# Kernel optimization log

Hardware: AMD Instinct MI355X
Metric: run time of the kernel (lower is better)

## Reference

```python
import jax, jax.numpy as jnp
import numpy as np

B, F, H, E, V, T = 128, 2048, 1024, 512, 16384, 20
TEMP = 1.0


def setup_inputs() -> dict:
    key = jax.random.key(0)
    ks = jax.random.split(key, 12)
    sc = lambda i, shape, s=0.02: jax.random.normal(ks[i], shape, jnp.float32) * s
    # Gumbel(0,1) noise for RelaxedOneHotCategorical.rsample
    u = jax.random.uniform(ks[11], (T, B, V), jnp.float32, 1e-6, 1.0 - 1e-6)
    gumbel = -jnp.log(-jnp.log(u))
    return dict(
        image_features=jax.random.normal(ks[0], (B, F), jnp.float32),
        agent_w=sc(1, (H, F)),
        agent_b=jnp.zeros((H,), jnp.float32),
        w_ih=sc(2, (3 * H, E)),
        w_hh=sc(3, (3 * H, H)),
        b_ih=jnp.zeros((3 * H,), jnp.float32),
        b_hh=jnp.zeros((3 * H,), jnp.float32),
        w_out=sc(4, (V, H)),
        b_out=jnp.zeros((V,), jnp.float32),
        emb_w=sc(5, (E, V)),
        sos=sc(6, (E,), 0.01),
        gumbel=gumbel,
    )


def _gru_cell(x, h, w_ih, w_hh, b_ih, b_hh):
    # torch.nn.GRUCell math
    gi = x @ w_ih.T + b_ih          # [B, 3H]
    gh = h @ w_hh.T + b_hh          # [B, 3H]
    i_r, i_z, i_n = jnp.split(gi, 3, axis=-1)
    h_r, h_z, h_n = jnp.split(gh, 3, axis=-1)
    r = jax.nn.sigmoid(i_r + h_r)
    z = jax.nn.sigmoid(i_z + h_z)
    n = jnp.tanh(i_n + r * h_n)
    return (1.0 - z) * n + z * h


def reference(image_features, agent_w, agent_b, w_ih, w_hh, b_ih, b_hh,
              w_out, b_out, emb_w, sos, gumbel):
    h0 = image_features @ agent_w.T + agent_b                 # agent: [B, H]
    e0 = jnp.broadcast_to(sos, (image_features.shape[0], sos.shape[0]))  # SOS embed

    def step(carry, g_t):
        h, e = carry
        h = _gru_cell(e, h, w_ih, w_hh, b_ih, b_hh)            # [B, H]
        logits = h @ w_out.T + b_out                           # [B, V]
        # Gumbel-softmax sample (training mode, not straight-through)
        x = jax.nn.softmax((logits + g_t) / TEMP, axis=-1)     # [B, V]
        e = x @ emb_w.T                                        # soft-one-hot embedding, [B, E]
        return (h, e), x

    _, seq = jax.lax.scan(step, (h0, e0), gumbel)              # [T, B, V]
    return jnp.transpose(seq, (1, 0, 2))                       # [B, T, V]
```

## Files before the change

### kernel.cpp

```cpp
#include <hip/hip_runtime.h>
#include <hip/hip_bf16.h>
#include <math.h>

namespace {

constexpr int kB = 128, kF = 2048, kH = 1024, kE = 512, kV = 16384, kT = 20;

typedef __attribute__((ext_vector_type(4))) float f32x4;
typedef __attribute__((ext_vector_type(8))) short bf16x8;

#define MFMA(a, b, c) __builtin_amdgcn_mfma_f32_16x16x32_bf16((a), (b), (c), 0, 0, 0)

__device__ __forceinline__ short f2bf(float f) {
  union { float f; unsigned u; } un;
  un.f = f;
  unsigned x = un.u;
  x += 0x7fffu + ((x >> 16) & 1u);
  return (short)(x >> 16);
}

__device__ __forceinline__ float bf2f(short s) {
  union { unsigned u; float f; } un;
  un.u = ((unsigned)(unsigned short)s) << 16;
  return un.f;
}

__device__ __forceinline__ float sigm(float x) { return 1.0f / (1.0f + __expf(-x)); }

__device__ __forceinline__ void cvt4(const float* __restrict__ s, short* __restrict__ d,
                                     long n4, long gid, long gs) {
  for (long i = gid; i < n4; i += gs) {
    float4 v = ((const float4*)s)[i];
    short4 o;
    o.x = f2bf(v.x); o.y = f2bf(v.y); o.z = f2bf(v.z); o.w = f2bf(v.w);
    ((short4*)d)[i] = o;
  }
}

__global__ __launch_bounds__(256) void k_convert(
    const float* __restrict__ wout, const float* __restrict__ emb,
    const float* __restrict__ wih, const float* __restrict__ whh,
    const float* __restrict__ aw, const float* __restrict__ img,
    const float* __restrict__ sos,
    short* __restrict__ wout_b, short* __restrict__ emb_b,
    short* __restrict__ wih_b, short* __restrict__ whh_b,
    short* __restrict__ aw_b, short* __restrict__ img_b,
    short* __restrict__ e0_b) {
  long gid = (long)blockIdx.x * blockDim.x + threadIdx.x;
  long gs = (long)gridDim.x * blockDim.x;
  cvt4(wout, wout_b, (long)kV * kH / 4, gid, gs);
  cvt4(emb, emb_b, (long)kE * kV / 4, gid, gs);
  cvt4(wih, wih_b, (long)3 * kH * kE / 4, gid, gs);
  cvt4(whh, whh_b, (long)3 * kH * kH / 4, gid, gs);
  cvt4(aw, aw_b, (long)kH * kF / 4, gid, gs);
  cvt4(img, img_b, (long)kB * kF / 4, gid, gs);
  for (long i = gid; i < kB * kE; i += gs) e0_b[i] = f2bf(sos[i & (kE - 1)]);
}

__global__ __launch_bounds__(256) void k_h0(const short* __restrict__ img_b,
                                            const short* __restrict__ aw_b,
                                            const float* __restrict__ ab,
                                            float* __restrict__ hf, short* __restrict__ hb) {
  int tid = threadIdx.x;
  int l = tid & 63, w = tid >> 6;
  int lr = l & 15, g = l >> 4, lk = g * 8;
  int col0 = blockIdx.x * 16;
  int row0 = w * 32;
  f32x4 acc[2] = {};
#pragma unroll 4
  for (int k0 = 0; k0 < kF; k0 += 32) {
    bf16x8 a0 = *(const bf16x8*)&img_b[(row0 + lr) * kF + k0 + lk];
    bf16x8 a1 = *(const bf16x8*)&img_b[(row0 + 16 + lr) * kF + k0 + lk];
    bf16x8 b = *(const bf16x8*)&aw_b[(size_t)(col0 + lr) * kF + k0 + lk];
    acc[0] = MFMA(a0, b, acc[0]);
    acc[1] = MFMA(a1, b, acc[1]);
  }
  int col = col0 + lr;
  float bias = ab[col];
#pragma unroll
  for (int mf = 0; mf < 2; ++mf)
#pragma unroll
    for (int j = 0; j < 4; ++j) {
      int row = row0 + mf * 16 + g * 4 + j;
      float v = acc[mf][j] + bias;
      hf[row * kH + col] = v;
      hb[row * kH + col] = f2bf(v);
    }
}

__global__ __launch_bounds__(256) void k_gru(
    const short* __restrict__ e_b, const short* __restrict__ hb_prev,
    float* __restrict__ hf,
    const short* __restrict__ wih_b, const short* __restrict__ whh_b,
    const float* __restrict__ bih, const float* __restrict__ bhh,
    short* __restrict__ hb_next, float* __restrict__ denom) {
  int tid = threadIdx.x;
  int l = tid & 63, w = tid >> 6;
  int lr = l & 15, g = l >> 4, lk = g * 8;
  int colt = blockIdx.x >> 1, half = blockIdx.x & 1;
  int col0 = colt * 16;
  int row0 = half * 64 + w * 16;
  if (blockIdx.x == 0 && tid < 32) {
    float4 z = {0.0f, 0.0f, 0.0f, 0.0f};
    *(float4*)&denom[tid * 4] = z;
  }
  f32x4 air = {}, aiz = {}, ain = {};
  f32x4 ahr = {}, ahz = {}, ahn = {};
#pragma unroll 8
  for (int k0 = 0; k0 < kE; k0 += 32) {
    bf16x8 a = *(const bf16x8*)&e_b[(row0 + lr) * kE + k0 + lk];
    bf16x8 br = *(const bf16x8*)&wih_b[(size_t)(col0 + lr) * kE + k0 + lk];
    bf16x8 bz = *(const bf16x8*)&wih_b[(size_t)(kH + col0 + lr) * kE + k0 + lk];
    bf16x8 bn = *(const bf16x8*)&wih_b[(size_t)(2 * kH + col0 + lr) * kE + k0 + lk];
    air = MFMA(a, br, air);
    aiz = MFMA(a, bz, aiz);
    ain = MFMA(a, bn, ain);
  }
#pragma unroll 8
  for (int k0 = 0; k0 < kH; k0 += 32) {
    bf16x8 a = *(const bf16x8*)&hb_prev[(row0 + lr) * kH + k0 + lk];
    bf16x8 br = *(const bf16x8*)&whh_b[(size_t)(col0 + lr) * kH + k0 + lk];
    bf16x8 bz = *(const bf16x8*)&whh_b[(size_t)(kH + col0 + lr) * kH + k0 + lk];
    bf16x8 bn = *(const bf16x8*)&whh_b[(size_t)(2 * kH + col0 + lr) * kH + k0 + lk];
    ahr = MFMA(a, br, ahr);
    ahz = MFMA(a, bz, ahz);
    ahn = MFMA(a, bn, ahn);
  }
  int col = col0 + lr;
  float bihr = bih[col], bhhr = bhh[col];
  float bihz = bih[kH + col], bhhz = bhh[kH + col];
  float bihn = bih[2 * kH + col], bhhn = bhh[2 * kH + col];
#pragma unroll
  for (int j = 0; j < 4; ++j) {
    int row = row0 + g * 4 + j;
    float r = sigm(air[j] + ahr[j] + bihr + bhhr);
    float z = sigm(aiz[j] + ahz[j] + bihz + bhhz);
    float nn = tanhf(ain[j] + bihn + r * (ahn[j] + bhhn));
    float hv = (1.0f - z) * nn + z * hf[row * kH + col];
    hf[row * kH + col] = hv;
    hb_next[row * kH + col] = f2bf(hv);
  }
}

__global__ __launch_bounds__(512) void k_logits(
    const short* __restrict__ h_b, const short* __restrict__ wout_b,
    const float* __restrict__ bout, const float* __restrict__ gum_t,
    short* __restrict__ p_b, float* __restrict__ denom) {
  int tid = threadIdx.x;
  int l = tid & 63, w = tid >> 6;
  int lr = l & 15, g = l >> 4, lk = g * 8;
  int wm = w >> 2, wn = w & 3;
  int n0 = blockIdx.x * 64;
  int col = n0 + wn * 16 + lr;
  int row0 = wm * 64;
  float gum[16];
#pragma unroll
  for (int mf = 0; mf < 4; ++mf)
#pragma unroll
    for (int j = 0; j < 4; ++j)
      gum[mf * 4 + j] = gum_t[(size_t)(row0 + mf * 16 + g * 4 + j) * kV + col];
  float bo = bout[col];
  const short* Bp = &wout_b[(size_t)col * kH + lk];
  f32x4 acc[4] = {};
  bf16x8 brg[8], arg[2][4];
#pragma unroll
  for (int k = 0; k < 8; ++k) brg[k] = *(const bf16x8*)(Bp + k * 32);
#pragma unroll
  for (int k = 0; k < 2; ++k)
#pragma unroll
    for (int mf = 0; mf < 4; ++mf)
      arg[k][mf] = *(const bf16x8*)&h_b[(row0 + mf * 16 + lr) * kH + k * 32 + lk];
#pragma unroll
  for (int k = 0; k < 32; ++k) {
    acc[0] = MFMA(arg[k & 1][0], brg[k & 7], acc[0]);
    acc[1] = MFMA(arg[k & 1][1], brg[k & 7], acc[1]);
    acc[2] = MFMA(arg[k & 1][2], brg[k & 7], acc[2]);
    acc[3] = MFMA(arg[k & 1][3], brg[k & 7], acc[3]);
    if (k < 24) brg[k & 7] = *(const bf16x8*)(Bp + (k + 8) * 32);
    if (k < 30) {
#pragma unroll
      for (int mf = 0; mf < 4; ++mf)
        arg[k & 1][mf] =
            *(const bf16x8*)&h_b[(row0 + mf * 16 + lr) * kH + (k + 2) * 32 + lk];
    }
  }
  __shared__ float ls[2][4][64];
  float p[16];
#pragma unroll
  for (int i = 0; i < 16; ++i) p[i] = __expf(acc[i >> 2][i & 3] + bo + gum[i]);
#pragma unroll
  for (int i = 0; i < 16; ++i) {
    int rl = (i >> 2) * 16 + g * 4 + (i & 3);
    p_b[(size_t)(row0 + rl) * kV + col] = f2bf(p[i]);
  }
#pragma unroll
  for (int i = 0; i < 16; ++i) {
    float s = p[i];
#pragma unroll
    for (int sf = 1; sf < 16; sf <<= 1) s += __shfl_xor(s, sf, 64);
    if (lr == 0) ls[wm][wn][(i >> 2) * 16 + g * 4 + (i & 3)] = s;
  }
  __syncthreads();
  if (tid < 128) {
    int row = tid, wmm = tid >> 6, rl = tid & 63;
    float sb = ls[wmm][0][rl] + ls[wmm][1][rl] + ls[wmm][2][rl] + ls[wmm][3][rl];
    atomicAdd(&denom[row], sb);
  }
}

__global__ __launch_bounds__(512) void k_e(
    const short* __restrict__ p_b, const float* __restrict__ denom,
    const short* __restrict__ emb_b, float* __restrict__ outp,
    float* __restrict__ epart) {
  int tid = threadIdx.x;
  int l = tid & 63, w = tid >> 6;
  int lr = l & 15, g = l >> 4, lk = g * 8;
  int wm = w >> 2, wn = w & 3;
  int kc = blockIdx.x >> 3, et = blockIdx.x & 7;
  int kbase = kc * 512;
  int colB = et * 64 + wn * 16 + lr;
  __shared__ float s_rd[kB];
  if (tid < kB) s_rd[tid] = 1.0f / denom[tid];
  __shared__ bf16x8 xs8[2048];
  char* xs = (char*)xs8;
  int colg = tid & 15, rrow = tid >> 4;
  f32x4 acc[4] = {};
  __syncthreads();
  for (int s = 0; s < 4; ++s) {
    if (s) __syncthreads();
#pragma unroll
    for (int rr = 0; rr < 4; ++rr) {
      int row = rr * 32 + rrow;
      int cb = s * 128 + colg * 8;
      bf16x8 p8 = *(const bf16x8*)&p_b[(size_t)row * kV + kbase + cb];
      float scl = s_rd[row];
      float f[8];
#pragma unroll
      for (int i = 0; i < 8; ++i) f[i] = bf2f(p8[i]) * scl;
      if (et == 0) {
        float4 o0, o1;
        o0.x = f[0]; o0.y = f[1]; o0.z = f[2]; o0.w = f[3];
        o1.x = f[4]; o1.y = f[5]; o1.z = f[6]; o1.w = f[7];
        *(float4*)&outp[(size_t)row * (kT * kV) + kbase + cb] = o0;
        *(float4*)&outp[(size_t)row * (kT * kV) + kbase + cb + 4] = o1;
      }
      bf16x8 xv;
#pragma unroll
      for (int i = 0; i < 8; ++i) xv[i] = f2bf(f[i]);
      unsigned off = (unsigned)(row * 256 + colg * 16) ^ ((row & 7) << 4);
      *(bf16x8*)(xs + off) = xv;
    }
    __syncthreads();
#pragma unroll
    for (int kk = 0; kk < 4; ++kk) {
      bf16x8 b = *(const bf16x8*)&emb_b[(size_t)colB * kV + kbase + s * 128 + kk * 32 + lk];
#pragma unroll
      for (int mf = 0; mf < 4; ++mf) {
        int rowa = wm * 64 + mf * 16 + lr;
        unsigned off = (unsigned)(rowa * 256 + (kk * 32 + lk) * 2) ^ ((rowa & 7) << 4);
        bf16x8 a = *(const bf16x8*)(xs + off);
        acc[mf] = MFMA(a, b, acc[mf]);
      }
    }
  }
#pragma unroll
  for (int mf = 0; mf < 4; ++mf)
#pragma unroll
    for (int j = 0; j < 4; ++j) {
      int row = wm * 64 + mf * 16 + g * 4 + j;
      epart[((size_t)kc * kB + row) * kE + et * 64 + wn * 16 + lr] = acc[mf][j];
    }
}

__global__ __launch_bounds__(256) void k_ereduce(const float* __restrict__ epart,
                                                 short* __restrict__ e_b) {
  int i = blockIdx.x * 256 + threadIdx.x;
  float s = 0.0f;
#pragma unroll
  for (int k = 0; k < 32; ++k) s += epart[(size_t)k * (kB * kE) + i];
  e_b[i] = f2bf(s);
}

}

extern "C" void kernel_launch(void* const* d_in, const int* in_sizes, int n_in,
                              void* d_out, int out_size, void* d_ws, size_t ws_size,
                              hipStream_t stream) {
  const float* img = (const float*)d_in[0];
  const float* aw = (const float*)d_in[1];
  const float* ab = (const float*)d_in[2];
  const float* wih = (const float*)d_in[3];
  const float* whh = (const float*)d_in[4];
  const float* bih = (const float*)d_in[5];
  const float* bhh = (const float*)d_in[6];
  const float* wout = (const float*)d_in[7];
  const float* bout = (const float*)d_in[8];
  const float* emb = (const float*)d_in[9];
  const float* sos = (const float*)d_in[10];
  const float* gum = (const float*)d_in[11];
  float* out = (float*)d_out;
  char* ws = (char*)d_ws;

  short* wout_b = (short*)(ws + 0);
  short* emb_b = (short*)(ws + 33554432);
  short* wih_b = (short*)(ws + 50331648);
  short* whh_b = (short*)(ws + 53477376);
  short* aw_b = (short*)(ws + 59768832);
  short* img_b = (short*)(ws + 63963136);
  float* hf = (float*)(ws + 64487424);
  short* hb0 = (short*)(ws + 65011712);
  short* hb1 = (short*)(ws + 65273856);
  short* e_b = (short*)(ws + 65536000);
  short* p_b = (short*)(ws + 65667072);
  float* denom = (float*)(ws + 69861376);
  float* epart = (float*)(ws + 69865472);

  short* hb[2] = {hb0, hb1};

  k_convert<<<2048, 256, 0, stream>>>(wout, emb, wih, whh, aw, img, sos, wout_b, emb_b,
                                      wih_b, whh_b, aw_b, img_b, e_b);
  k_h0<<<64, 256, 0, stream>>>(img_b, aw_b, ab, hf, hb[0]);
  for (int t = 0; t < kT; ++t) {
    int rp = t & 1, wp = rp ^ 1;
    float* outp = out + (size_t)t * kV;
    k_gru<<<128, 256, 0, stream>>>(e_b, hb[rp], hf, wih_b, whh_b, bih, bhh, hb[wp],
                                   denom);
    k_logits<<<256, 512, 0, stream>>>(hb[wp], wout_b, bout, gum + (size_t)t * kB * kV,
                                      p_b, denom);
    k_e<<<256, 512, 0, stream>>>(p_b, denom, emb_b, outp, epart);
    k_ereduce<<<256, 256, 0, stream>>>(epart, e_b);
  }
}
```

Before: 1.937 ms.

## Fuse per-timestep GRU, logits and embedding kernels into one cooperative persistent kernel

Replaces the four kernels launched per timestep with a single cooperative kernel that loops over all timesteps and separates the phases with grid-wide syncs. This removes about 80 kernel launches and their launch gaps. The GRU phase now splits K across warps and reduces the partials in shared memory, which gives 256 blocks instead of 128. The embedding phase accumulates with float atomics into an fp32 e buffer, so the separate partial-reduce kernel goes away, and blocks 128-255 write the normalized output rows in parallel. The cost is grid-sync latency, float-atomic contention, and a nondeterministic summation order.

```diff
diff --git a/kernel.cpp b/kernel.cpp
--- a/kernel.cpp
+++ b/kernel.cpp
@@ -1,6 +1,9 @@
 #include <hip/hip_runtime.h>
 #include <hip/hip_bf16.h>
+#include <hip/hip_cooperative_groups.h>
 #include <math.h>
+
+namespace cg = cooperative_groups;
 
 namespace {
 
@@ -45,7 +48,7 @@
     short* __restrict__ wout_b, short* __restrict__ emb_b,
     short* __restrict__ wih_b, short* __restrict__ whh_b,
     short* __restrict__ aw_b, short* __restrict__ img_b,
-    short* __restrict__ e0_b) {
+    float* __restrict__ e_f) {
   long gid = (long)blockIdx.x * blockDim.x + threadIdx.x;
   long gs = (long)gridDim.x * blockDim.x;
   cvt4(wout, wout_b, (long)kV * kH / 4, gid, gs);
@@ -54,7 +57,7 @@
   cvt4(whh, whh_b, (long)3 * kH * kH / 4, gid, gs);
   cvt4(aw, aw_b, (long)kH * kF / 4, gid, gs);
   cvt4(img, img_b, (long)kB * kF / 4, gid, gs);
-  for (long i = gid; i < kB * kE; i += gs) e0_b[i] = f2bf(sos[i & (kE - 1)]);
+  for (long i = gid; i < kB * kE; i += gs) e_f[i] = sos[i & (kE - 1)];
 }
 
 __global__ __launch_bounds__(256) void k_h0(const short* __restrict__ img_b,
@@ -88,197 +91,225 @@
     }
 }
 
-__global__ __launch_bounds__(256) void k_gru(
-    const short* __restrict__ e_b, const short* __restrict__ hb_prev,
-    float* __restrict__ hf,
+__global__ __launch_bounds__(512, 2) void k_main(
     const short* __restrict__ wih_b, const short* __restrict__ whh_b,
     const float* __restrict__ bih, const float* __restrict__ bhh,
-    short* __restrict__ hb_next, float* __restrict__ denom) {
-  int tid = threadIdx.x;
+    const short* __restrict__ wout_b, const float* __restrict__ bout,
+    const float* __restrict__ gum, const short* __restrict__ emb_b,
+    float* __restrict__ e_f, float* __restrict__ hf,
+    short* __restrict__ hb0, short* __restrict__ hb1,
+    short* __restrict__ p_b, float* __restrict__ denom, float* __restrict__ out) {
+  cg::grid_group gg = cg::this_grid();
+  __shared__ f32x4 smem4[2080];
+  int bid = blockIdx.x, tid = threadIdx.x;
   int l = tid & 63, w = tid >> 6;
   int lr = l & 15, g = l >> 4, lk = g * 8;
-  int colt = blockIdx.x >> 1, half = blockIdx.x & 1;
-  int col0 = colt * 16;
-  int row0 = half * 64 + w * 16;
-  if (blockIdx.x == 0 && tid < 32) {
-    float4 z = {0.0f, 0.0f, 0.0f, 0.0f};
-    *(float4*)&denom[tid * 4] = z;
+
+  for (int t = 0; t < kT; ++t) {
+    const short* hbp = (t & 1) ? hb1 : hb0;
+    short* hbn = (t & 1) ? hb0 : hb1;
+    const float* gum_t = gum + (size_t)t * kB * kV;
+
+    {
+      if (bid == 0 && tid < 32) {
+        float4 z = {0.0f, 0.0f, 0.0f, 0.0f};
+        *(float4*)&denom[tid * 4] = z;
+      }
+      int colt = bid >> 2, rq = bid & 3;
+      int col0 = colt * 16;
+      int rh = w & 1, kq = w >> 1;
+      int row0 = rq * 32 + rh * 16;
+      f32x4 pr = {}, pz = {}, pin = {}, phn = {};
+      int ke0 = kq * 128;
+#pragma unroll
+      for (int ki = 0; ki < 4; ++ki) {
+        int k0 = ke0 + ki * 32;
+        float4 af0 = *(const float4*)&e_f[(row0 + lr) * kE + k0 + lk];
+        float4 af1 = *(const float4*)&e_f[(row0 + lr) * kE + k0 + lk + 4];
+        bf16x8 a;
+        a[0] = f2bf(af0.x); a[1] = f2bf(af0.y); a[2] = f2bf(af0.z); a[3] = f2bf(af0.w);
+        a[4] = f2bf(af1.x); a[5] = f2bf(af1.y); a[6] = f2bf(af1.z); a[7] = f2bf(af1.w);
+        bf16x8 br = *(const bf16x8*)&wih_b[(size_t)(col0 + lr) * kE + k0 + lk];
+        bf16x8 bz = *(const bf16x8*)&wih_b[(size_t)(kH + col0 + lr) * kE + k0 + lk];
+        bf16x8 bn = *(const bf16x8*)&wih_b[(size_t)(2 * kH + col0 + lr) * kE + k0 + lk];
+        pr = MFMA(a, br, pr);
+        pz = MFMA(a, bz, pz);
+        pin = MFMA(a, bn, pin);
+      }
+      int kh0 = kq * 256;
+#pragma unroll
+      for (int ki = 0; ki < 8; ++ki) {
+        int k0 = kh0 + ki * 32;
+        bf16x8 a = *(const bf16x8*)&hbp[(row0 + lr) * kH + k0 + lk];
+        bf16x8 br = *(const bf16x8*)&whh_b[(size_t)(col0 + lr) * kH + k0 + lk];
+        bf16x8 bz = *(const bf16x8*)&whh_b[(size_t)(kH + col0 + lr) * kH + k0 + lk];
+        bf16x8 bn = *(const bf16x8*)&whh_b[(size_t)(2 * kH + col0 + lr) * kH + k0 + lk];
+        pr = MFMA(a, br, pr);
+        pz = MFMA(a, bz, pz);
+        phn = MFMA(a, bn, phn);
+      }
+      smem4[((0 * 2 + rh) * 4 + kq) * 64 + l] = pr;
+      smem4[((1 * 2 + rh) * 4 + kq) * 64 + l] = pz;
+      smem4[((2 * 2 + rh) * 4 + kq) * 64 + l] = pin;
+      smem4[((3 * 2 + rh) * 4 + kq) * 64 + l] = phn;
+      __syncthreads();
+      if (w < 2) {
+        int rh2 = w;
+        int row0e = rq * 32 + rh2 * 16;
+        f32x4 rs = {}, zs = {}, is = {}, hs = {};
+#pragma unroll
+        for (int q = 0; q < 4; ++q) {
+          rs += smem4[((0 * 2 + rh2) * 4 + q) * 64 + l];
+          zs += smem4[((1 * 2 + rh2) * 4 + q) * 64 + l];
+          is += smem4[((2 * 2 + rh2) * 4 + q) * 64 + l];
+          hs += smem4[((3 * 2 + rh2) * 4 + q) * 64 + l];
+        }
+        int col = col0 + lr;
+        float bihr = bih[col], bhhr = bhh[col];
+        float bihz = bih[kH + col], bhhz = bhh[kH + col];
+        float bihn = bih[2 * kH + col], bhhn = bhh[2 * kH + col];
+#pragma unroll
+        for (int j = 0; j < 4; ++j) {
+          int row = row0e + g * 4 + j;
+          float r = sigm(rs[j] + bihr + bhhr);
+          float z = sigm(zs[j] + bihz + bhhz);
+          float nn = tanhf(is[j] + bihn + r * (hs[j] + bhhn));
+          float hv = (1.0f - z) * nn + z * hf[row * kH + col];
+          hf[row * kH + col] = hv;
+          hbn[row * kH + col] = f2bf(hv);
+        }
+      }
+    }
+    gg.sync();
+
+    {
+      int gi = bid * 512 + tid;
+      if (gi < kB * kE) e_f[gi] = 0.0f;
+      int wm = w >> 2, wn = w & 3;
+      int col = bid * 64 + wn * 16 + lr;
+      int row0 = wm * 64;
+      float gmr[16];
+#pragma unroll
+      for (int mf = 0; mf < 4; ++mf)
+#pragma unroll
+        for (int j = 0; j < 4; ++j)
+          gmr[mf * 4 + j] = gum_t[(size_t)(row0 + mf * 16 + g * 4 + j) * kV + col];
+      float bo = bout[col];
+      const short* Bp = &wout_b[(size_t)col * kH + lk];
+      f32x4 acc[4] = {};
+      bf16x8 brg[8], arg[2][4];
+#pragma unroll
+      for (int k = 0; k < 8; ++k) brg[k] = *(const bf16x8*)(Bp + k * 32);
+#pragma unroll
+      for (int k = 0; k < 2; ++k)
+#pragma unroll
+        for (int mf = 0; mf < 4; ++mf)
+          arg[k][mf] = *(const bf16x8*)&hbn[(row0 + mf * 16 + lr) * kH + k * 32 + lk];
+#pragma unroll
+      for (int k = 0; k < 32; ++k) {
+        acc[0] = MFMA(arg[k & 1][0], brg[k & 7], acc[0]);
+        acc[1] = MFMA(arg[k & 1][1], brg[k & 7], acc[1]);
+        acc[2] = MFMA(arg[k & 1][2], brg[k & 7], acc[2]);
+        acc[3] = MFMA(arg[k & 1][3], brg[k & 7], acc[3]);
+        if (k < 24) brg[k & 7] = *(const bf16x8*)(Bp + (k + 8) * 32);
+        if (k < 30) {
+#pragma unroll
+          for (int mf = 0; mf < 4; ++mf)
+            arg[k & 1][mf] =
+                *(const bf16x8*)&hbn[(row0 + mf * 16 + lr) * kH + (k + 2) * 32 + lk];
+        }
+      }
+      float* ls = (float*)smem4;
+      float p[16];
+#pragma unroll
+      for (int i = 0; i < 16; ++i) p[i] = __expf(acc[i >> 2][i & 3] + bo + gmr[i]);
+#pragma unroll
+      for (int i = 0; i < 16; ++i) {
+        int rl = (i >> 2) * 16 + g * 4 + (i & 3);
+        p_b[(size_t)(row0 + rl) * kV + col] = f2bf(p[i]);
+      }
+#pragma unroll
+      for (int i = 0; i < 16; ++i) {
+        float s = p[i];
+#pragma unroll
+        for (int sf = 1; sf < 16; sf <<= 1) s += __shfl_xor(s, sf, 64);
+        if (lr == 0) ls[((wm * 4 + wn) * 64) + (i >> 2) * 16 + g * 4 + (i & 3)] = s;
+      }
+      __syncthreads();
+      if (tid < 128) {
+        int row = tid, wmm = tid >> 6, rl = tid & 63;
+        float sb = ls[(wmm * 4 + 0) * 64 + rl] + ls[(wmm * 4 + 1) * 64 + rl] +
+                   ls[(wmm * 4 + 2) * 64 + rl] + ls[(wmm * 4 + 3) * 64 + rl];
+        atomicAdd(&denom[row], sb);
+      }
+    }
+    gg.sync();
+
+    if (bid < 128) {
+      int wm = w >> 2, wn = w & 3;
+      int kc = bid >> 3, et = bid & 7;
+      int kbase = kc * 1024;
+      int colB = et * 64 + wn * 16 + lr;
+      float* s_rd = (float*)smem4;
+      char* xs = (char*)(smem4 + 32);
+      if (tid < kB) s_rd[tid] = 1.0f / denom[tid];
+      int colg = tid & 15, rrow = tid >> 4;
+      f32x4 acc[4] = {};
+      __syncthreads();
+      for (int s = 0; s < 8; ++s) {
+        if (s) __syncthreads();
+#pragma unroll
+        for (int rr = 0; rr < 4; ++rr) {
+          int row = rr * 32 + rrow;
+          int cb = s * 128 + colg * 8;
+          bf16x8 p8 = *(const bf16x8*)&p_b[(size_t)row * kV + kbase + cb];
+          float scl = s_rd[row];
+          bf16x8 xv;
+#pragma unroll
+          for (int i = 0; i < 8; ++i) xv[i] = f2bf(bf2f(p8[i]) * scl);
+          unsigned off = (unsigned)(row * 256 + colg * 16) ^ ((row & 7) << 4);
+          *(bf16x8*)(xs + off) = xv;
+        }
+        __syncthreads();
+#pragma unroll
+        for (int kk = 0; kk < 4; ++kk) {
+          bf16x8 b =
+              *(const bf16x8*)&emb_b[(size_t)colB * kV + kbase + s * 128 + kk * 32 + lk];
+#pragma unroll
+          for (int mf = 0; mf < 4; ++mf) {
+            int rowa = wm * 64 + mf * 16 + lr;
+            unsigned off = (unsigned)(rowa * 256 + (kk * 32 + lk) * 2) ^ ((rowa & 7) << 4);
+            bf16x8 a = *(const bf16x8*)(xs + off);
+            acc[mf] = MFMA(a, b, acc[mf]);
+          }
+        }
+      }
+#pragma unroll
+      for (int mf = 0; mf < 4; ++mf)
+#pragma unroll
+        for (int j = 0; j < 4; ++j) {
+          int row = wm * 64 + mf * 16 + g * 4 + j;
+          atomicAdd(&e_f[row * kE + et * 64 + wn * 16 + lr], acc[mf][j]);
+        }
+    } else {
+      int r = bid - 128;
+      float rd = 1.0f / denom[r];
+      const short* pr = &p_b[(size_t)r * kV + tid * 32];
+      float* orow = &out[(size_t)r * (kT * kV) + (size_t)t * kV + tid * 32];
+#pragma unroll
+      for (int jj = 0; jj < 4; ++jj) {
+        bf16x8 p8 = *(const bf16x8*)(pr + jj * 8);
+        float4 o0, o1;
+        o0.x = bf2f(p8[0]) * rd; o0.y = bf2f(p8[1]) * rd;
+        o0.z = bf2f(p8[2]) * rd; o0.w = bf2f(p8[3]) * rd;
+        o1.x = bf2f(p8[4]) * rd; o1.y = bf2f(p8[5]) * rd;
+        o1.z = bf2f(p8[6]) * rd; o1.w = bf2f(p8[7]) * rd;
+        *(float4*)(orow + jj * 8) = o0;
+        *(float4*)(orow + jj * 8 + 4) = o1;
+      }
+    }
+    if (t < kT - 1) gg.sync();
   }
-  f32x4 air = {}, aiz = {}, ain = {};
-  f32x4 ahr = {}, ahz = {}, ahn = {};
-#pragma unroll 8
-  for (int k0 = 0; k0 < kE; k0 += 32) {
-    bf16x8 a = *(const bf16x8*)&e_b[(row0 + lr) * kE + k0 + lk];
-    bf16x8 br = *(const bf16x8*)&wih_b[(size_t)(col0 + lr) * kE + k0 + lk];
-    bf16x8 bz = *(const bf16x8*)&wih_b[(size_t)(kH + col0 + lr) * kE + k0 + lk];
-    bf16x8 bn = *(const bf16x8*)&wih_b[(size_t)(2 * kH + col0 + lr) * kE + k0 + lk];
-    air = MFMA(a, br, air);
-    aiz = MFMA(a, bz, aiz);
-    ain = MFMA(a, bn, ain);
-  }
-#pragma unroll 8
-  for (int k0 = 0; k0 < kH; k0 += 32) {
-    bf16x8 a = *(const bf16x8*)&hb_prev[(row0 + lr) * kH + k0 + lk];
-    bf16x8 br = *(const bf16x8*)&whh_b[(size_t)(col0 + lr) * kH + k0 + lk];
-    bf16x8 bz = *(const bf16x8*)&whh_b[(size_t)(kH + col0 + lr) * kH + k0 + lk];
-    bf16x8 bn = *(const bf16x8*)&whh_b[(size_t)(2 * kH + col0 + lr) * kH + k0 + lk];
-    ahr = MFMA(a, br, ahr);
-    ahz = MFMA(a, bz, ahz);
-    ahn = MFMA(a, bn, ahn);
-  }
-  int col = col0 + lr;
-  float bihr = bih[col], bhhr = bhh[col];
-  float bihz = bih[kH + col], bhhz = bhh[kH + col];
-  float bihn = bih[2 * kH + col], bhhn = bhh[2 * kH + col];
-#pragma unroll
-  for (int j = 0; j < 4; ++j) {
-    int row = row0 + g * 4 + j;
-    float r = sigm(air[j] + ahr[j] + bihr + bhhr);
-    float z = sigm(aiz[j] + ahz[j] + bihz + bhhz);
-    float nn = tanhf(ain[j] + bihn + r * (ahn[j] + bhhn));
-    float hv = (1.0f - z) * nn + z * hf[row * kH + col];
-    hf[row * kH + col] = hv;
-    hb_next[row * kH + col] = f2bf(hv);
-  }
-}
-
-__global__ __launch_bounds__(512) void k_logits(
-    const short* __restrict__ h_b, const short* __restrict__ wout_b,
-    const float* __restrict__ bout, const float* __restrict__ gum_t,
-    short* __restrict__ p_b, float* __restrict__ denom) {
-  int tid = threadIdx.x;
-  int l = tid & 63, w = tid >> 6;
-  int lr = l & 15, g = l >> 4, lk = g * 8;
-  int wm = w >> 2, wn = w & 3;
-  int n0 = blockIdx.x * 64;
-  int col = n0 + wn * 16 + lr;
-  int row0 = wm * 64;
-  float gum[16];
-#pragma unroll
-  for (int mf = 0; mf < 4; ++mf)
-#pragma unroll
-    for (int j = 0; j < 4; ++j)
-      gum[mf * 4 + j] = gum_t[(size_t)(row0 + mf * 16 + g * 4 + j) * kV + col];
-  float bo = bout[col];
-  const short* Bp = &wout_b[(size_t)col * kH + lk];
-  f32x4 acc[4] = {};
-  bf16x8 brg[8], arg[2][4];
-#pragma unroll
-  for (int k = 0; k < 8; ++k) brg[k] = *(const bf16x8*)(Bp + k * 32);
-#pragma unroll
-  for (int k = 0; k < 2; ++k)
-#pragma unroll
-    for (int mf = 0; mf < 4; ++mf)
-      arg[k][mf] = *(const bf16x8*)&h_b[(row0 + mf * 16 + lr) * kH + k * 32 + lk];
-#pragma unroll
-  for (int k = 0; k < 32; ++k) {
-    acc[0] = MFMA(arg[k & 1][0], brg[k & 7], acc[0]);
-    acc[1] = MFMA(arg[k & 1][1], brg[k & 7], acc[1]);
-    acc[2] = MFMA(arg[k & 1][2], brg[k & 7], acc[2]);
-    acc[3] = MFMA(arg[k & 1][3], brg[k & 7], acc[3]);
-    if (k < 24) brg[k & 7] = *(const bf16x8*)(Bp + (k + 8) * 32);
-    if (k < 30) {
-#pragma unroll
-      for (int mf = 0; mf < 4; ++mf)
-        arg[k & 1][mf] =
-            *(const bf16x8*)&h_b[(row0 + mf * 16 + lr) * kH + (k + 2) * 32 + lk];
-    }
-  }
-  __shared__ float ls[2][4][64];
-  float p[16];
-#pragma unroll
-  for (int i = 0; i < 16; ++i) p[i] = __expf(acc[i >> 2][i & 3] + bo + gum[i]);
-#pragma unroll
-  for (int i = 0; i < 16; ++i) {
-    int rl = (i >> 2) * 16 + g * 4 + (i & 3);
-    p_b[(size_t)(row0 + rl) * kV + col] = f2bf(p[i]);
-  }
-#pragma unroll
-  for (int i = 0; i < 16; ++i) {
-    float s = p[i];
-#pragma unroll
-    for (int sf = 1; sf < 16; sf <<= 1) s += __shfl_xor(s, sf, 64);
-    if (lr == 0) ls[wm][wn][(i >> 2) * 16 + g * 4 + (i & 3)] = s;
-  }
-  __syncthreads();
-  if (tid < 128) {
-    int row = tid, wmm = tid >> 6, rl = tid & 63;
-    float sb = ls[wmm][0][rl] + ls[wmm][1][rl] + ls[wmm][2][rl] + ls[wmm][3][rl];
-    atomicAdd(&denom[row], sb);
-  }
-}
-
-__global__ __launch_bounds__(512) void k_e(
-    const short* __restrict__ p_b, const float* __restrict__ denom,
-    const short* __restrict__ emb_b, float* __restrict__ outp,
-    float* __restrict__ epart) {
-  int tid = threadIdx.x;
-  int l = tid & 63, w = tid >> 6;
-  int lr = l & 15, g = l >> 4, lk = g * 8;
-  int wm = w >> 2, wn = w & 3;
-  int kc = blockIdx.x >> 3, et = blockIdx.x & 7;
-  int kbase = kc * 512;
-  int colB = et * 64 + wn * 16 + lr;
-  __shared__ float s_rd[kB];
-  if (tid < kB) s_rd[tid] = 1.0f / denom[tid];
-  __shared__ bf16x8 xs8[2048];
-  char* xs = (char*)xs8;
-  int colg = tid & 15, rrow = tid >> 4;
-  f32x4 acc[4] = {};
-  __syncthreads();
-  for (int s = 0; s < 4; ++s) {
-    if (s) __syncthreads();
-#pragma unroll
-    for (int rr = 0; rr < 4; ++rr) {
-      int row = rr * 32 + rrow;
-      int cb = s * 128 + colg * 8;
-      bf16x8 p8 = *(const bf16x8*)&p_b[(size_t)row * kV + kbase + cb];
-      float scl = s_rd[row];
-      float f[8];
-#pragma unroll
-      for (int i = 0; i < 8; ++i) f[i] = bf2f(p8[i]) * scl;
-      if (et == 0) {
-        float4 o0, o1;
-        o0.x = f[0]; o0.y = f[1]; o0.z = f[2]; o0.w = f[3];
-        o1.x = f[4]; o1.y = f[5]; o1.z = f[6]; o1.w = f[7];
-        *(float4*)&outp[(size_t)row * (kT * kV) + kbase + cb] = o0;
-        *(float4*)&outp[(size_t)row * (kT * kV) + kbase + cb + 4] = o1;
-      }
-      bf16x8 xv;
-#pragma unroll
-      for (int i = 0; i < 8; ++i) xv[i] = f2bf(f[i]);
-      unsigned off = (unsigned)(row * 256 + colg * 16) ^ ((row & 7) << 4);
-      *(bf16x8*)(xs + off) = xv;
-    }
-    __syncthreads();
-#pragma unroll
-    for (int kk = 0; kk < 4; ++kk) {
-      bf16x8 b = *(const bf16x8*)&emb_b[(size_t)colB * kV + kbase + s * 128 + kk * 32 + lk];
-#pragma unroll
-      for (int mf = 0; mf < 4; ++mf) {
-        int rowa = wm * 64 + mf * 16 + lr;
-        unsigned off = (unsigned)(rowa * 256 + (kk * 32 + lk) * 2) ^ ((rowa & 7) << 4);
-        bf16x8 a = *(const bf16x8*)(xs + off);
-        acc[mf] = MFMA(a, b, acc[mf]);
-      }
-    }
-  }
-#pragma unroll
-  for (int mf = 0; mf < 4; ++mf)
-#pragma unroll
-    for (int j = 0; j < 4; ++j) {
-      int row = wm * 64 + mf * 16 + g * 4 + j;
-      epart[((size_t)kc * kB + row) * kE + et * 64 + wn * 16 + lr] = acc[mf][j];
-    }
-}
-
-__global__ __launch_bounds__(256) void k_ereduce(const float* __restrict__ epart,
-                                                 short* __restrict__ e_b) {
-  int i = blockIdx.x * 256 + threadIdx.x;
-  float s = 0.0f;
-#pragma unroll
-  for (int k = 0; k < 32; ++k) s += epart[(size_t)k * (kB * kE) + i];
-  e_b[i] = f2bf(s);
 }
 
 }
@@ -310,24 +341,17 @@
   float* hf = (float*)(ws + 64487424);
   short* hb0 = (short*)(ws + 65011712);
   short* hb1 = (short*)(ws + 65273856);
-  short* e_b = (short*)(ws + 65536000);
-  short* p_b = (short*)(ws + 65667072);
-  float* denom = (float*)(ws + 69861376);
-  float* epart = (float*)(ws + 69865472);
-
-  short* hb[2] = {hb0, hb1};
+  short* p_b = (short*)(ws + 65536000);
+  float* denom = (float*)(ws + 69730304);
+  float* e_f = (float*)(ws + 69734400);
 
   k_convert<<<2048, 256, 0, stream>>>(wout, emb, wih, whh, aw, img, sos, wout_b, emb_b,
-                                      wih_b, whh_b, aw_b, img_b, e_b);
-  k_h0<<<64, 256, 0, stream>>>(img_b, aw_b, ab, hf, hb[0]);
-  for (int t = 0; t < kT; ++t) {
-    int rp = t & 1, wp = rp ^ 1;
-    float* outp = out + (size_t)t * kV;
-    k_gru<<<128, 256, 0, stream>>>(e_b, hb[rp], hf, wih_b, whh_b, bih, bhh, hb[wp],
-                                   denom);
-    k_logits<<<256, 512, 0, stream>>>(hb[wp], wout_b, bout, gum + (size_t)t * kB * kV,
-                                      p_b, denom);
-    k_e<<<256, 512, 0, stream>>>(p_b, denom, emb_b, outp, epart);
-    k_ereduce<<<256, 256, 0, stream>>>(epart, e_b);
-  }
-}
+                                      wih_b, whh_b, aw_b, img_b, e_f);
+  k_h0<<<64, 256, 0, stream>>>(img_b, aw_b, ab, hf, hb0);
+
+  void* args[] = {(void*)&wih_b, (void*)&whh_b, (void*)&bih,   (void*)&bhh,
+                  (void*)&wout_b, (void*)&bout, (void*)&gum,   (void*)&emb_b,
+                  (void*)&e_f,    (void*)&hf,   (void*)&hb0,   (void*)&hb1,
+                  (void*)&p_b,    (void*)&denom, (void*)&out};
+  hipLaunchCooperativeKernel((void*)k_main, dim3(256), dim3(512), args, 0, stream);
+}
```

Result: slower. 3.719 ms (+92.0%).

## Overlap output writes with GRU, split-K GRU, atomic embedding reduction

Applied to the files above, without the earlier changes.

Moves the normalized-probability output write out of the embedding kernel and into spare waves of the next step's GRU kernel, with a final k_out for the last step. Denominators are double-buffered so this overlap is safe. The GRU kernel now splits K across waves and reduces the partial sums through shared memory, which doubles the block count. The embedding partials are accumulated with float atomics into an fp32 buffer that the logits kernel zeroes, replacing the separate reduce kernel and one launch per step. The trade-off is atomic contention, summation order that is no longer deterministic, and reliance on p_b staying intact until the next GRU kernel reads it.

```diff
diff --git a/kernel.cpp b/kernel.cpp
--- a/kernel.cpp
+++ b/kernel.cpp
@@ -45,7 +45,7 @@
     short* __restrict__ wout_b, short* __restrict__ emb_b,
     short* __restrict__ wih_b, short* __restrict__ whh_b,
     short* __restrict__ aw_b, short* __restrict__ img_b,
-    short* __restrict__ e0_b) {
+    float* __restrict__ e_f) {
   long gid = (long)blockIdx.x * blockDim.x + threadIdx.x;
   long gs = (long)gridDim.x * blockDim.x;
   cvt4(wout, wout_b, (long)kV * kH / 4, gid, gs);
@@ -54,7 +54,7 @@
   cvt4(whh, whh_b, (long)3 * kH * kH / 4, gid, gs);
   cvt4(aw, aw_b, (long)kH * kF / 4, gid, gs);
   cvt4(img, img_b, (long)kB * kF / 4, gid, gs);
-  for (long i = gid; i < kB * kE; i += gs) e0_b[i] = f2bf(sos[i & (kE - 1)]);
+  for (long i = gid; i < kB * kE; i += gs) e_f[i] = sos[i & (kE - 1)];
 }
 
 __global__ __launch_bounds__(256) void k_h0(const short* __restrict__ img_b,
@@ -88,64 +88,119 @@
     }
 }
 
-__global__ __launch_bounds__(256) void k_gru(
-    const short* __restrict__ e_b, const short* __restrict__ hb_prev,
+__global__ __launch_bounds__(512) void k_gru(
+    const float* __restrict__ e_f, const short* __restrict__ hb_prev,
     float* __restrict__ hf,
     const short* __restrict__ wih_b, const short* __restrict__ whh_b,
     const float* __restrict__ bih, const float* __restrict__ bhh,
-    short* __restrict__ hb_next, float* __restrict__ denom) {
-  int tid = threadIdx.x;
+    short* __restrict__ hb_next, float* __restrict__ denom_cur,
+    const short* __restrict__ p_prev, const float* __restrict__ denom_prev,
+    float* __restrict__ out_prev) {
+  int tid = threadIdx.x, bid = blockIdx.x;
   int l = tid & 63, w = tid >> 6;
   int lr = l & 15, g = l >> 4, lk = g * 8;
-  int colt = blockIdx.x >> 1, half = blockIdx.x & 1;
+  __shared__ f32x4 part[4][2][2][64];
+  int colt = bid >> 2, rq = bid & 3;
   int col0 = colt * 16;
-  int row0 = half * 64 + w * 16;
-  if (blockIdx.x == 0 && tid < 32) {
-    float4 z = {0.0f, 0.0f, 0.0f, 0.0f};
-    *(float4*)&denom[tid * 4] = z;
-  }
-  f32x4 air = {}, aiz = {}, ain = {};
-  f32x4 ahr = {}, ahz = {}, ahn = {};
-#pragma unroll 8
-  for (int k0 = 0; k0 < kE; k0 += 32) {
-    bf16x8 a = *(const bf16x8*)&e_b[(row0 + lr) * kE + k0 + lk];
-    bf16x8 br = *(const bf16x8*)&wih_b[(size_t)(col0 + lr) * kE + k0 + lk];
-    bf16x8 bz = *(const bf16x8*)&wih_b[(size_t)(kH + col0 + lr) * kE + k0 + lk];
-    bf16x8 bn = *(const bf16x8*)&wih_b[(size_t)(2 * kH + col0 + lr) * kE + k0 + lk];
-    air = MFMA(a, br, air);
-    aiz = MFMA(a, bz, aiz);
-    ain = MFMA(a, bn, ain);
-  }
-#pragma unroll 8
-  for (int k0 = 0; k0 < kH; k0 += 32) {
-    bf16x8 a = *(const bf16x8*)&hb_prev[(row0 + lr) * kH + k0 + lk];
-    bf16x8 br = *(const bf16x8*)&whh_b[(size_t)(col0 + lr) * kH + k0 + lk];
-    bf16x8 bz = *(const bf16x8*)&whh_b[(size_t)(kH + col0 + lr) * kH + k0 + lk];
-    bf16x8 bn = *(const bf16x8*)&whh_b[(size_t)(2 * kH + col0 + lr) * kH + k0 + lk];
-    ahr = MFMA(a, br, ahr);
-    ahz = MFMA(a, bz, ahz);
-    ahn = MFMA(a, bn, ahn);
-  }
-  int col = col0 + lr;
-  float bihr = bih[col], bhhr = bhh[col];
-  float bihz = bih[kH + col], bhhz = bhh[kH + col];
-  float bihn = bih[2 * kH + col], bhhn = bhh[2 * kH + col];
-#pragma unroll
-  for (int j = 0; j < 4; ++j) {
-    int row = row0 + g * 4 + j;
-    float r = sigm(air[j] + ahr[j] + bihr + bhhr);
-    float z = sigm(aiz[j] + ahz[j] + bihz + bhhz);
-    float nn = tanhf(ain[j] + bihn + r * (ahn[j] + bhhn));
-    float hv = (1.0f - z) * nn + z * hf[row * kH + col];
-    hf[row * kH + col] = hv;
-    hb_next[row * kH + col] = f2bf(hv);
+  if (w < 4) {
+    int rh = w & 1, kq = w >> 1;
+    int row0 = rq * 32 + rh * 16;
+    if (bid == 0 && tid < 32) {
+      f32x4 z = {0.0f, 0.0f, 0.0f, 0.0f};
+      *(f32x4*)&denom_cur[tid * 4] = z;
+    }
+    f32x4 ar = {}, az = {}, ain = {}, ahn = {};
+    if (kq == 0) {
+#pragma unroll 4
+      for (int ki = 0; ki < 16; ++ki) {
+        int k0 = ki * 32;
+        float4 af0 = *(const float4*)&e_f[(row0 + lr) * kE + k0 + lk];
+        float4 af1 = *(const float4*)&e_f[(row0 + lr) * kE + k0 + lk + 4];
+        bf16x8 a;
+        a[0] = f2bf(af0.x); a[1] = f2bf(af0.y); a[2] = f2bf(af0.z); a[3] = f2bf(af0.w);
+        a[4] = f2bf(af1.x); a[5] = f2bf(af1.y); a[6] = f2bf(af1.z); a[7] = f2bf(af1.w);
+        bf16x8 br = *(const bf16x8*)&wih_b[(size_t)(col0 + lr) * kE + k0 + lk];
+        bf16x8 bz = *(const bf16x8*)&wih_b[(size_t)(kH + col0 + lr) * kE + k0 + lk];
+        bf16x8 bn = *(const bf16x8*)&wih_b[(size_t)(2 * kH + col0 + lr) * kE + k0 + lk];
+        ar = MFMA(a, br, ar);
+        az = MFMA(a, bz, az);
+        ain = MFMA(a, bn, ain);
+      }
+#pragma unroll 4
+      for (int ki = 0; ki < 8; ++ki) {
+        int k0 = ki * 32;
+        bf16x8 a = *(const bf16x8*)&hb_prev[(row0 + lr) * kH + k0 + lk];
+        bf16x8 br = *(const bf16x8*)&whh_b[(size_t)(col0 + lr) * kH + k0 + lk];
+        bf16x8 bz = *(const bf16x8*)&whh_b[(size_t)(kH + col0 + lr) * kH + k0 + lk];
+        bf16x8 bn = *(const bf16x8*)&whh_b[(size_t)(2 * kH + col0 + lr) * kH + k0 + lk];
+        ar = MFMA(a, br, ar);
+        az = MFMA(a, bz, az);
+        ahn = MFMA(a, bn, ahn);
+      }
+    } else {
+#pragma unroll 4
+      for (int ki = 0; ki < 24; ++ki) {
+        int k0 = 256 + ki * 32;
+        bf16x8 a = *(const bf16x8*)&hb_prev[(row0 + lr) * kH + k0 + lk];
+        bf16x8 br = *(const bf16x8*)&whh_b[(size_t)(col0 + lr) * kH + k0 + lk];
+        bf16x8 bz = *(const bf16x8*)&whh_b[(size_t)(kH + col0 + lr) * kH + k0 + lk];
+        bf16x8 bn = *(const bf16x8*)&whh_b[(size_t)(2 * kH + col0 + lr) * kH + k0 + lk];
+        ar = MFMA(a, br, ar);
+        az = MFMA(a, bz, az);
+        ahn = MFMA(a, bn, ahn);
+      }
+    }
+    part[0][rh][kq][l] = ar;
+    part[1][rh][kq][l] = az;
+    part[2][rh][kq][l] = ain;
+    part[3][rh][kq][l] = ahn;
+  } else if (out_prev != nullptr) {
+    int r = bid >> 1, halfc = bid & 1;
+    float rd = 1.0f / denom_prev[r];
+    int coff = halfc * 8192 + (w - 4) * 2048 + l * 32;
+    const short* pr = p_prev + (size_t)r * kV + coff;
+    float* orow = out_prev + (size_t)r * (kT * kV) + coff;
+#pragma unroll
+    for (int jj = 0; jj < 4; ++jj) {
+      bf16x8 p8 = *(const bf16x8*)(pr + jj * 8);
+      f32x4 o0, o1;
+      o0[0] = bf2f(p8[0]) * rd; o0[1] = bf2f(p8[1]) * rd;
+      o0[2] = bf2f(p8[2]) * rd; o0[3] = bf2f(p8[3]) * rd;
+      o1[0] = bf2f(p8[4]) * rd; o1[1] = bf2f(p8[5]) * rd;
+      o1[2] = bf2f(p8[6]) * rd; o1[3] = bf2f(p8[7]) * rd;
+      __builtin_nontemporal_store(o0, (f32x4*)(orow + jj * 8));
+      __builtin_nontemporal_store(o1, (f32x4*)(orow + jj * 8 + 4));
+    }
+  }
+  __syncthreads();
+  if (w < 2) {
+    int rh2 = w;
+    int row0e = rq * 32 + rh2 * 16;
+    f32x4 rs = part[0][rh2][0][l] + part[0][rh2][1][l];
+    f32x4 zs = part[1][rh2][0][l] + part[1][rh2][1][l];
+    f32x4 is = part[2][rh2][0][l] + part[2][rh2][1][l];
+    f32x4 hs = part[3][rh2][0][l] + part[3][rh2][1][l];
+    int col = col0 + lr;
+    float bihr = bih[col], bhhr = bhh[col];
+    float bihz = bih[kH + col], bhhz = bhh[kH + col];
+    float bihn = bih[2 * kH + col], bhhn = bhh[2 * kH + col];
+#pragma unroll
+    for (int j = 0; j < 4; ++j) {
+      int row = row0e + g * 4 + j;
+      float r = sigm(rs[j] + bihr + bhhr);
+      float z = sigm(zs[j] + bihz + bhhz);
+      float nn = tanhf(is[j] + bihn + r * (hs[j] + bhhn));
+      float hv = (1.0f - z) * nn + z * hf[row * kH + col];
+      hf[row * kH + col] = hv;
+      hb_next[row * kH + col] = f2bf(hv);
+    }
   }
 }
 
 __global__ __launch_bounds__(512) void k_logits(
     const short* __restrict__ h_b, const short* __restrict__ wout_b,
     const float* __restrict__ bout, const float* __restrict__ gum_t,
-    short* __restrict__ p_b, float* __restrict__ denom) {
+    short* __restrict__ p_b, float* __restrict__ denom, float* __restrict__ e_f) {
   int tid = threadIdx.x;
   int l = tid & 63, w = tid >> 6;
   int lr = l & 15, g = l >> 4, lk = g * 8;
@@ -153,12 +208,15 @@
   int n0 = blockIdx.x * 64;
   int col = n0 + wn * 16 + lr;
   int row0 = wm * 64;
-  float gum[16];
+  int gi = blockIdx.x * 512 + tid;
+  if (gi < kB * kE) e_f[gi] = 0.0f;
+  float gmr[16];
 #pragma unroll
   for (int mf = 0; mf < 4; ++mf)
 #pragma unroll
     for (int j = 0; j < 4; ++j)
-      gum[mf * 4 + j] = gum_t[(size_t)(row0 + mf * 16 + g * 4 + j) * kV + col];
+      gmr[mf * 4 + j] = __builtin_nontemporal_load(
+          &gum_t[(size_t)(row0 + mf * 16 + g * 4 + j) * kV + col]);
   float bo = bout[col];
   const short* Bp = &wout_b[(size_t)col * kH + lk];
   f32x4 acc[4] = {};
@@ -187,7 +245,7 @@
   __shared__ float ls[2][4][64];
   float p[16];
 #pragma unroll
-  for (int i = 0; i < 16; ++i) p[i] = __expf(acc[i >> 2][i & 3] + bo + gum[i]);
+  for (int i = 0; i < 16; ++i) p[i] = __expf(acc[i >> 2][i & 3] + bo + gmr[i]);
 #pragma unroll
   for (int i = 0; i < 16; ++i) {
     int rl = (i >> 2) * 16 + g * 4 + (i & 3);
@@ -210,8 +268,7 @@
 
 __global__ __launch_bounds__(512) void k_e(
     const short* __restrict__ p_b, const float* __restrict__ denom,
-    const short* __restrict__ emb_b, float* __restrict__ outp,
-    float* __restrict__ epart) {
+    const short* __restrict__ emb_b, float* __restrict__ e_f) {
   int tid = threadIdx.x;
   int l = tid & 63, w = tid >> 6;
   int lr = l & 15, g = l >> 4, lk = g * 8;
@@ -234,19 +291,9 @@
       int cb = s * 128 + colg * 8;
       bf16x8 p8 = *(const bf16x8*)&p_b[(size_t)row * kV + kbase + cb];
       float scl = s_rd[row];
-      float f[8];
-#pragma unroll
-      for (int i = 0; i < 8; ++i) f[i] = bf2f(p8[i]) * scl;
-      if (et == 0) {
-        float4 o0, o1;
-        o0.x = f[0]; o0.y = f[1]; o0.z = f[2]; o0.w = f[3];
-        o1.x = f[4]; o1.y = f[5]; o1.z = f[6]; o1.w = f[7];
-        *(float4*)&outp[(size_t)row * (kT * kV) + kbase + cb] = o0;
-        *(float4*)&outp[(size_t)row * (kT * kV) + kbase + cb + 4] = o1;
-      }
       bf16x8 xv;
 #pragma unroll
-      for (int i = 0; i < 8; ++i) xv[i] = f2bf(f[i]);
+      for (int i = 0; i < 8; ++i) xv[i] = f2bf(bf2f(p8[i]) * scl);
       unsigned off = (unsigned)(row * 256 + colg * 16) ^ ((row & 7) << 4);
       *(bf16x8*)(xs + off) = xv;
     }
@@ -268,17 +315,30 @@
 #pragma unroll
     for (int j = 0; j < 4; ++j) {
       int row = wm * 64 + mf * 16 + g * 4 + j;
-      epart[((size_t)kc * kB + row) * kE + et * 64 + wn * 16 + lr] = acc[mf][j];
-    }
-}
-
-__global__ __launch_bounds__(256) void k_ereduce(const float* __restrict__ epart,
-                                                 short* __restrict__ e_b) {
-  int i = blockIdx.x * 256 + threadIdx.x;
-  float s = 0.0f;
-#pragma unroll
-  for (int k = 0; k < 32; ++k) s += epart[(size_t)k * (kB * kE) + i];
-  e_b[i] = f2bf(s);
+      atomicAdd(&e_f[row * kE + et * 64 + wn * 16 + lr], acc[mf][j]);
+    }
+}
+
+__global__ __launch_bounds__(256) void k_out(const short* __restrict__ p_b,
+                                             const float* __restrict__ denom,
+                                             float* __restrict__ outp) {
+  int tid = threadIdx.x, bid = blockIdx.x;
+  int r = bid >> 1, halfc = bid & 1;
+  float rd = 1.0f / denom[r];
+  int coff = halfc * 8192 + tid * 32;
+  const short* pr = p_b + (size_t)r * kV + coff;
+  float* orow = outp + (size_t)r * (kT * kV) + coff;
+#pragma unroll
+  for (int jj = 0; jj < 4; ++jj) {
+    bf16x8 p8 = *(const bf16x8*)(pr + jj * 8);
+    f32x4 o0, o1;
+    o0[0] = bf2f(p8[0]) * rd; o0[1] = bf2f(p8[1]) * rd;
+    o0[2] = bf2f(p8[2]) * rd; o0[3] = bf2f(p8[3]) * rd;
+    o1[0] = bf2f(p8[4]) * rd; o1[1] = bf2f(p8[5]) * rd;
+    o1[2] = bf2f(p8[6]) * rd; o1[3] = bf2f(p8[7]) * rd;
+    __builtin_nontemporal_store(o0, (f32x4*)(orow + jj * 8));
+    __builtin_nontemporal_store(o1, (f32x4*)(orow + jj * 8 + 4));
+  }
 }
 
 }
@@ -310,24 +370,25 @@
   float* hf = (float*)(ws + 64487424);
   short* hb0 = (short*)(ws + 65011712);
   short* hb1 = (short*)(ws + 65273856);
-  short* e_b = (short*)(ws + 65536000);
-  short* p_b = (short*)(ws + 65667072);
-  float* denom = (float*)(ws + 69861376);
-  float* epart = (float*)(ws + 69865472);
+  short* p_b = (short*)(ws + 65536000);
+  float* denoms = (float*)(ws + 69730304);
+  float* e_f = (float*)(ws + 69732352);
 
   short* hb[2] = {hb0, hb1};
 
   k_convert<<<2048, 256, 0, stream>>>(wout, emb, wih, whh, aw, img, sos, wout_b, emb_b,
-                                      wih_b, whh_b, aw_b, img_b, e_b);
+                                      wih_b, whh_b, aw_b, img_b, e_f);
   k_h0<<<64, 256, 0, stream>>>(img_b, aw_b, ab, hf, hb[0]);
   for (int t = 0; t < kT; ++t) {
     int rp = t & 1, wp = rp ^ 1;
-    float* outp = out + (size_t)t * kV;
-    k_gru<<<128, 256, 0, stream>>>(e_b, hb[rp], hf, wih_b, whh_b, bih, bhh, hb[wp],
-                                   denom);
+    float* denomC = denoms + (t & 1) * 256;
+    float* denomP = denoms + ((t & 1) ^ 1) * 256;
+    float* out_prev = (t == 0) ? nullptr : out + (size_t)(t - 1) * kV;
+    k_gru<<<256, 512, 0, stream>>>(e_f, hb[rp], hf, wih_b, whh_b, bih, bhh, hb[wp],
+                                   denomC, p_b, denomP, out_prev);
     k_logits<<<256, 512, 0, stream>>>(hb[wp], wout_b, bout, gum + (size_t)t * kB * kV,
-                                      p_b, denom);
-    k_e<<<256, 512, 0, stream>>>(p_b, denom, emb_b, outp, epart);
-    k_ereduce<<<256, 256, 0, stream>>>(epart, e_b);
-  }
-}
+                                      p_b, denomC, e_f);
+    k_e<<<256, 512, 0, stream>>>(p_b, denomC, emb_b, e_f);
+  }
+  k_out<<<256, 256, 0, stream>>>(p_b, denoms + 256, out + (size_t)(kT - 1) * kV);
+}
```

Result: faster. 1.896 ms (-2.1%).
